# Optimization experiments

Measured on AMD Instinct MI355X. Metric: run time of the kernel, lower is better.

Reference implementation:

```python
import jax, jax.numpy as jnp
import numpy as np

N = 30        # samples per bezier curve
W = 60        # output image side
LENGTH = 160  # curves per sample
ALPHA = 2e-4  # gaussian splat bandwidth
VIEWBOX = (0.0, 0.0, 1.0, 1.0)
BATCH = 128


def _bezier_T(n):
    # matches the torch buffer: reparametrized t, then (reordered) Bernstein basis
    t = jnp.arange(n, dtype=jnp.float32) / n
    t = 2.0 * t**3 - 3.0 * t**2 + 2.0 * t
    t3 = t**3
    return jnp.stack([t3,
                      3.0 * (t**2 - t3),
                      3.0 * (t3 - 2.0 * t**2 + t),
                      (1.0 - t)**3], axis=1)  # [n, 4]


def setup_inputs() -> dict:
    key = jax.random.key(0)
    x = jax.random.uniform(key, (BATCH, LENGTH, 8), dtype=jnp.float32)
    return {"x": x}


def reference(x):
    B = x.shape[0]
    T = _bezier_T(N)                                   # [n, 4]
    board = jnp.arange(W, dtype=jnp.float32) / W       # [W]
    bX = board * VIEWBOX[2] + VIEWBOX[0]
    bY = board * VIEWBOX[3] + VIEWBOX[1]

    ctrl = x.reshape(B, LENGTH, 4, 2)
    pts = jnp.einsum('nk,blkc->blnc', T, ctrl)         # [B, L, n, 2] bezier samples
    X = pts[..., 0]                                    # [B, L, n]
    Y = pts[..., 1]

    # gaussian splat of each sampled point onto the pixel grid (separable)
    gX = jnp.exp(-jnp.square(bX[None, None, :, None] - X[:, :, None, :]) / ALPHA)  # [B, L, W, n]
    gY = jnp.exp(-jnp.square(bY[None, None, :, None] - Y[:, :, None, :]) / ALPHA)  # [B, L, W, n]

    # outer-product over the two axes, reduced over samples n and curves L
    res = jnp.einsum('blwn,blvn->bwv', gX, gY)         # [B, W, W]
    return jnp.minimum(res, 1.0)
```

## Files before the change

### kernel.cpp

```cpp
#include <hip/hip_runtime.h>


namespace {
constexpr int   kN = 30;
constexpr int   kW = 60;
constexpr int   kL = 160;
constexpr int   kB = 128;
constexpr float kAlphaInv = 5000.0f;
constexpr float kRadPix = 3.5f;
constexpr int   KSPLIT = 4;
constexpr int   CPB = kL / KSPLIT;
constexpr int   KPC = 32;
constexpr int   KBLK = CPB * KPC;
constexpr int   KC = 128;
constexpr int   NCH = KBLK / KC;
constexpr int   LDK = KC + 8;
constexpr int   kPix = kW * kW;
}

using f32x4 = __attribute__((ext_vector_type(4))) float;
using f16x8 = __attribute__((ext_vector_type(8))) _Float16;

__global__ __launch_bounds__(256, 2) void bezier_gemm_kernel(const float* __restrict__ x,
                                                             float* __restrict__ partial) {
  __shared__ _Float16 sh[2][64][LDK];
  const int b   = blockIdx.x / KSPLIT;
  const int ks  = blockIdx.x % KSPLIT;
  const int tid = threadIdx.x;
  const int lane = tid & 63;
  const int wid  = tid >> 6;
  const int wi = wid >> 1;
  const int vi = wid & 1;
  const int l15 = lane & 15;
  const int l4  = lane >> 4;

  f32x4 acc4[2][2] = {};

  const float* xb = x + ((size_t)b * kL + (size_t)ks * CPB) * 8;

  {
    uint4* shv = (uint4*)&sh[0][0][0];
    constexpr int NZ = 2 * 64 * LDK * 2 / 16;
    for (int i = tid; i < NZ; i += 256) shv[i] = make_uint4(0, 0, 0, 0);
  }

  const int col = tid & 127;
  const int mat = tid >> 7;
  const int n   = col & (KPC - 1);
  const bool valid = (n < kN);
  float B0, B1, B2, B3;
  {
    float t0 = (float)n * (1.0f / 30.0f);
    float t  = 2.0f * t0 * t0 * t0 - 3.0f * t0 * t0 + 2.0f * t0;
    float t2 = t * t, t3 = t2 * t;
    B0 = t3;
    B1 = 3.0f * (t2 - t3);
    B2 = 3.0f * (t3 - 2.0f * t2 + t);
    float omt = 1.0f - t;
    B3 = omt * omt * omt;
  }
  int lo_prev = 0;

  __syncthreads();

  for (int ch = 0; ch < NCH; ++ch) {
    if (valid) {
      const int lc = ch * 4 + (col >> 5);
      const float4* c = (const float4*)(xb + lc * 8);
      float4 c0 = c[0], c1 = c[1];
      float P = mat ? (B0 * c0.y + B1 * c0.w + B2 * c1.y + B3 * c1.w)
                    : (B0 * c0.x + B1 * c0.z + B2 * c1.x + B3 * c1.z);
      float fp = P * (float)kW;
      int lo = (int)ceilf(fp - kRadPix);
#pragma unroll
      for (int i = 0; i < 8; ++i) {
        int m = lo_prev + i;
        if (m >= 0 && m < kW) sh[mat][m][col] = (_Float16)0.0f;
      }
#pragma unroll
      for (int i = 0; i < 8; ++i) {
        int m = lo + i;
        float d = (float)m * (1.0f / 60.0f) - P;
        float e = __expf(-d * d * kAlphaInv);
        if (m >= 0 && m < kW) sh[mat][m][col] = (_Float16)e;
      }
      lo_prev = lo;
    }
    __syncthreads();

#pragma unroll
    for (int kk = 0; kk < KC; kk += 32) {
      const int ke = kk + l4 * 8;
      f16x8 a0 = *(const f16x8*)&sh[0][wi * 32 + l15][ke];
      f16x8 a1 = *(const f16x8*)&sh[0][wi * 32 + 16 + l15][ke];
      f16x8 b0 = *(const f16x8*)&sh[1][vi * 32 + l15][ke];
      f16x8 b1 = *(const f16x8*)&sh[1][vi * 32 + 16 + l15][ke];
      acc4[0][0] = __builtin_amdgcn_mfma_f32_16x16x32_f16(a0, b0, acc4[0][0], 0, 0, 0);
      acc4[0][1] = __builtin_amdgcn_mfma_f32_16x16x32_f16(a0, b1, acc4[0][1], 0, 0, 0);
      acc4[1][0] = __builtin_amdgcn_mfma_f32_16x16x32_f16(a1, b0, acc4[1][0], 0, 0, 0);
      acc4[1][1] = __builtin_amdgcn_mfma_f32_16x16x32_f16(a1, b1, acc4[1][1], 0, 0, 0);
    }
    __syncthreads();
  }

  float* pb = partial + (size_t)blockIdx.x * kPix;
#pragma unroll
  for (int mt = 0; mt < 2; ++mt) {
#pragma unroll
    for (int vt = 0; vt < 2; ++vt) {
      const int v = vi * 32 + vt * 16 + l15;
#pragma unroll
      for (int r = 0; r < 4; ++r) {
        const int w = wi * 32 + mt * 16 + l4 * 4 + r;
        if (w < kW && v < kW) pb[w * kW + v] = acc4[mt][vt][r];
      }
    }
  }
}

__global__ __launch_bounds__(256) void reduce_kernel(const float* __restrict__ partial,
                                                     float* __restrict__ out) {
  int i = blockIdx.x * 256 + threadIdx.x;
  if (i >= kB * kPix) return;
  int b = i / kPix;
  int j = i - b * kPix;
  const float* p = partial + (size_t)b * KSPLIT * kPix + j;
  float s = p[0] + p[kPix] + p[2 * kPix] + p[3 * kPix];
  out[i] = fminf(s, 1.0f);
}

__global__ __launch_bounds__(1024) void splat_direct_kernel(const float* __restrict__ x,
                                                            float* __restrict__ out) {
  __shared__ float res[kPix];
  const int b = blockIdx.x;
  const int tid = threadIdx.x;
  for (int i = tid; i < kPix; i += 1024) res[i] = 0.0f;
  __syncthreads();
  const float* xb = x + (size_t)b * kL * 8;
  for (int p = tid; p < kL * kN; p += 1024) {
    int l = p / kN;
    int n = p - l * kN;
    float t0 = (float)n * (1.0f / 30.0f);
    float t  = 2.0f * t0 * t0 * t0 - 3.0f * t0 * t0 + 2.0f * t0;
    float t2 = t * t, t3 = t2 * t;
    float B0 = t3, B1 = 3.0f * (t2 - t3), B2 = 3.0f * (t3 - 2.0f * t2 + t);
    float omt = 1.0f - t, B3 = omt * omt * omt;
    const float4* c = (const float4*)(xb + l * 8);
    float4 c0 = c[0], c1 = c[1];
    float X = B0 * c0.x + B1 * c0.z + B2 * c1.x + B3 * c1.z;
    float Y = B0 * c0.y + B1 * c0.w + B2 * c1.y + B3 * c1.w;
    float fx = X * kW, fy = Y * kW;
    int wlo = (int)ceilf(fx - kRadPix), vlo = (int)ceilf(fy - kRadPix);
    for (int i = 0; i < 8; ++i) {
      int w = wlo + i;
      if (w < 0 || w >= kW) continue;
      float dw = ((float)w - fx) * (1.0f / kW);
      float gx = __expf(-dw * dw * kAlphaInv);
      for (int j = 0; j < 8; ++j) {
        int v = vlo + j;
        if (v < 0 || v >= kW) continue;
        float dv = ((float)v - fy) * (1.0f / kW);
        atomicAdd(&res[w * kW + v], gx * __expf(-dv * dv * kAlphaInv));
      }
    }
  }
  __syncthreads();
  float* outb = out + (size_t)b * kPix;
  for (int i = tid; i < kPix; i += 1024) outb[i] = fminf(res[i], 1.0f);
}

extern "C" void kernel_launch(void* const* d_in, const int* in_sizes, int n_in,
                              void* d_out, int out_size, void* d_ws, size_t ws_size,
                              hipStream_t stream) {
  const float* x = (const float*)d_in[0];
  float* out = (float*)d_out;
  const size_t part_bytes = (size_t)kB * KSPLIT * kPix * sizeof(float);

  if (ws_size >= part_bytes) {
    float* partial = (float*)d_ws;
    bezier_gemm_kernel<<<dim3(kB * KSPLIT), dim3(256), 0, stream>>>(x, partial);
    int n = kB * kPix;
    reduce_kernel<<<dim3((n + 255) / 256), dim3(256), 0, stream>>>(partial, out);
  } else {
    splat_direct_kernel<<<dim3(kB), dim3(1024), 0, stream>>>(x, out);
  }
}
```

Measured before the change: 23.97 us.

## Fuse split-K GEMM and reduction into one block per batch with 32x32 MFMA

```diff
diff --git a/kernel.cpp b/kernel.cpp
--- a/kernel.cpp
+++ b/kernel.cpp
@@ -8,45 +8,37 @@
 constexpr int   kB = 128;
 constexpr float kAlphaInv = 5000.0f;
 constexpr float kRadPix = 3.5f;
-constexpr int   KSPLIT = 4;
-constexpr int   CPB = kL / KSPLIT;
-constexpr int   KPC = 32;
-constexpr int   KBLK = CPB * KPC;
-constexpr int   KC = 128;
-constexpr int   NCH = KBLK / KC;
-constexpr int   LDK = KC + 8;
+constexpr int   KC  = 256;
+constexpr int   NCH = kL * 32 / KC;
 constexpr int   kPix = kW * kW;
 }
 
-using f32x4 = __attribute__((ext_vector_type(4))) float;
-using f16x8 = __attribute__((ext_vector_type(8))) _Float16;
+using f32x16 = __attribute__((ext_vector_type(16))) float;
+using f16x8  = __attribute__((ext_vector_type(8))) _Float16;
 
-__global__ __launch_bounds__(256, 2) void bezier_gemm_kernel(const float* __restrict__ x,
-                                                             float* __restrict__ partial) {
-  __shared__ _Float16 sh[2][64][LDK];
-  const int b   = blockIdx.x / KSPLIT;
-  const int ks  = blockIdx.x % KSPLIT;
-  const int tid = threadIdx.x;
+__device__ __forceinline__ int lds_off(int mat, int row, int col) {
+  int g = ((col >> 3) ^ row) & 31;
+  g = ((col >> 3) & 24) | (((col >> 3) ^ row) & 7);
+  return ((mat << 6) + row) * KC + (g << 3) + (col & 7);
+}
+
+__global__ __launch_bounds__(512, 1) void bezier_fused_kernel(const float* __restrict__ x,
+                                                              float* __restrict__ out) {
+  __shared__ _Float16 sh[2 * 64 * KC];
+  const int b    = blockIdx.x;
+  const int tid  = threadIdx.x;
   const int lane = tid & 63;
   const int wid  = tid >> 6;
-  const int wi = wid >> 1;
-  const int vi = wid & 1;
-  const int l15 = lane & 15;
-  const int l4  = lane >> 4;
+  const int l31  = lane & 31;
+  const int hi   = lane >> 5;
 
-  f32x4 acc4[2][2] = {};
+  f32x16 acc[2][2] = {};
 
-  const float* xb = x + ((size_t)b * kL + (size_t)ks * CPB) * 8;
+  const float* xb = x + (size_t)b * kL * 8;
 
-  {
-    uint4* shv = (uint4*)&sh[0][0][0];
-    constexpr int NZ = 2 * 64 * LDK * 2 / 16;
-    for (int i = tid; i < NZ; i += 256) shv[i] = make_uint4(0, 0, 0, 0);
-  }
-
-  const int col = tid & 127;
-  const int mat = tid >> 7;
-  const int n   = col & (KPC - 1);
+  const int col = tid & 255;
+  const int mat = tid >> 8;
+  const int n   = col & 31;
   const bool valid = (n < kN);
   float B0, B1, B2, B3;
   {
@@ -59,13 +51,17 @@
     float omt = 1.0f - t;
     B3 = omt * omt * omt;
   }
-  int lo_prev = 0;
+  int lo_prev = -1000;
 
+  {
+    uint4* z = (uint4*)sh;
+    for (int i = tid; i < 2 * 64 * KC * 2 / 16; i += 512) z[i] = make_uint4(0, 0, 0, 0);
+  }
   __syncthreads();
 
   for (int ch = 0; ch < NCH; ++ch) {
     if (valid) {
-      const int lc = ch * 4 + (col >> 5);
+      const int lc = ch * 8 + (col >> 5);
       const float4* c = (const float4*)(xb + lc * 8);
       float4 c0 = c[0], c1 = c[1];
       float P = mat ? (B0 * c0.y + B1 * c0.w + B2 * c1.y + B3 * c1.w)
@@ -75,98 +71,77 @@
 #pragma unroll
       for (int i = 0; i < 8; ++i) {
         int m = lo_prev + i;
-        if (m >= 0 && m < kW) sh[mat][m][col] = (_Float16)0.0f;
+        if (m >= 0 && m < kW) sh[lds_off(mat, m, col)] = (_Float16)0.0f;
       }
 #pragma unroll
       for (int i = 0; i < 8; ++i) {
         int m = lo + i;
-        float d = (float)m * (1.0f / 60.0f) - P;
-        float e = __expf(-d * d * kAlphaInv);
-        if (m >= 0 && m < kW) sh[mat][m][col] = (_Float16)e;
+        if (m >= 0 && m < kW) {
+          float d = (float)m * (1.0f / 60.0f) - P;
+          sh[lds_off(mat, m, col)] = (_Float16)__expf(-d * d * kAlphaInv);
+        }
       }
       lo_prev = lo;
     }
     __syncthreads();
 
 #pragma unroll
-    for (int kk = 0; kk < KC; kk += 32) {
-      const int ke = kk + l4 * 8;
-      f16x8 a0 = *(const f16x8*)&sh[0][wi * 32 + l15][ke];
-      f16x8 a1 = *(const f16x8*)&sh[0][wi * 32 + 16 + l15][ke];
-      f16x8 b0 = *(const f16x8*)&sh[1][vi * 32 + l15][ke];
-      f16x8 b1 = *(const f16x8*)&sh[1][vi * 32 + 16 + l15][ke];
-      acc4[0][0] = __builtin_amdgcn_mfma_f32_16x16x32_f16(a0, b0, acc4[0][0], 0, 0, 0);
-      acc4[0][1] = __builtin_amdgcn_mfma_f32_16x16x32_f16(a0, b1, acc4[0][1], 0, 0, 0);
-      acc4[1][0] = __builtin_amdgcn_mfma_f32_16x16x32_f16(a1, b0, acc4[1][0], 0, 0, 0);
-      acc4[1][1] = __builtin_amdgcn_mfma_f32_16x16x32_f16(a1, b1, acc4[1][1], 0, 0, 0);
+    for (int ks = 0; ks < 2; ++ks) {
+      const int gb = wid * 4 + ks * 2 + hi;
+      const int ra = ((0 << 6) + l31) * KC + ((((gb ^ l31) & 7) | (gb & 24)) << 3);
+      const int rA = ((0 << 6) + 32 + l31) * KC + ((((gb ^ l31) & 7) | (gb & 24)) << 3);
+      const int rb = ((1 << 6) + l31) * KC + ((((gb ^ l31) & 7) | (gb & 24)) << 3);
+      const int rB = ((1 << 6) + 32 + l31) * KC + ((((gb ^ l31) & 7) | (gb & 24)) << 3);
+      f16x8 a0 = *(const f16x8*)&sh[ra];
+      f16x8 a1 = *(const f16x8*)&sh[rA];
+      f16x8 b0 = *(const f16x8*)&sh[rb];
+      f16x8 b1 = *(const f16x8*)&sh[rB];
+      acc[0][0] = __builtin_amdgcn_mfma_f32_32x32x16_f16(a0, b0, acc[0][0], 0, 0, 0);
+      acc[0][1] = __builtin_amdgcn_mfma_f32_32x32x16_f16(a0, b1, acc[0][1], 0, 0, 0);
+      acc[1][0] = __builtin_amdgcn_mfma_f32_32x32x16_f16(a1, b0, acc[1][0], 0, 0, 0);
+      acc[1][1] = __builtin_amdgcn_mfma_f32_32x32x16_f16(a1, b1, acc[1][1], 0, 0, 0);
     }
     __syncthreads();
   }
 
-  float* pb = partial + (size_t)blockIdx.x * kPix;
+  float* red = (float*)sh;
+  if (wid < 4) {
+    float* slot = red + wid * 4096;
 #pragma unroll
-  for (int mt = 0; mt < 2; ++mt) {
+    for (int mi = 0; mi < 2; ++mi)
 #pragma unroll
-    for (int vt = 0; vt < 2; ++vt) {
-      const int v = vi * 32 + vt * 16 + l15;
+      for (int vi = 0; vi < 2; ++vi)
 #pragma unroll
-      for (int r = 0; r < 4; ++r) {
-        const int w = wi * 32 + mt * 16 + l4 * 4 + r;
-        if (w < kW && v < kW) pb[w * kW + v] = acc4[mt][vt][r];
-      }
-    }
-  }
-}
-
-__global__ __launch_bounds__(256) void reduce_kernel(const float* __restrict__ partial,
-                                                     float* __restrict__ out) {
-  int i = blockIdx.x * 256 + threadIdx.x;
-  if (i >= kB * kPix) return;
-  int b = i / kPix;
-  int j = i - b * kPix;
-  const float* p = partial + (size_t)b * KSPLIT * kPix + j;
-  float s = p[0] + p[kPix] + p[2 * kPix] + p[3 * kPix];
-  out[i] = fminf(s, 1.0f);
-}
-
-__global__ __launch_bounds__(1024) void splat_direct_kernel(const float* __restrict__ x,
-                                                            float* __restrict__ out) {
-  __shared__ float res[kPix];
-  const int b = blockIdx.x;
-  const int tid = threadIdx.x;
-  for (int i = tid; i < kPix; i += 1024) res[i] = 0.0f;
-  __syncthreads();
-  const float* xb = x + (size_t)b * kL * 8;
-  for (int p = tid; p < kL * kN; p += 1024) {
-    int l = p / kN;
-    int n = p - l * kN;
-    float t0 = (float)n * (1.0f / 30.0f);
-    float t  = 2.0f * t0 * t0 * t0 - 3.0f * t0 * t0 + 2.0f * t0;
-    float t2 = t * t, t3 = t2 * t;
-    float B0 = t3, B1 = 3.0f * (t2 - t3), B2 = 3.0f * (t3 - 2.0f * t2 + t);
-    float omt = 1.0f - t, B3 = omt * omt * omt;
-    const float4* c = (const float4*)(xb + l * 8);
-    float4 c0 = c[0], c1 = c[1];
-    float X = B0 * c0.x + B1 * c0.z + B2 * c1.x + B3 * c1.z;
-    float Y = B0 * c0.y + B1 * c0.w + B2 * c1.y + B3 * c1.w;
-    float fx = X * kW, fy = Y * kW;
-    int wlo = (int)ceilf(fx - kRadPix), vlo = (int)ceilf(fy - kRadPix);
-    for (int i = 0; i < 8; ++i) {
-      int w = wlo + i;
-      if (w < 0 || w >= kW) continue;
-      float dw = ((float)w - fx) * (1.0f / kW);
-      float gx = __expf(-dw * dw * kAlphaInv);
-      for (int j = 0; j < 8; ++j) {
-        int v = vlo + j;
-        if (v < 0 || v >= kW) continue;
-        float dv = ((float)v - fy) * (1.0f / kW);
-        atomicAdd(&res[w * kW + v], gx * __expf(-dv * dv * kAlphaInv));
-      }
-    }
+        for (int r = 0; r < 16; ++r) {
+          int row = mi * 32 + (r & 3) + 8 * (r >> 2) + 4 * hi;
+          int cc  = vi * 32 + l31;
+          slot[row * 64 + cc] = acc[mi][vi][r];
+        }
   }
   __syncthreads();
-  float* outb = out + (size_t)b * kPix;
-  for (int i = tid; i < kPix; i += 1024) outb[i] = fminf(res[i], 1.0f);
+  if (wid >= 4) {
+    float* slot = red + (wid - 4) * 4096;
+#pragma unroll
+    for (int mi = 0; mi < 2; ++mi)
+#pragma unroll
+      for (int vi = 0; vi < 2; ++vi)
+#pragma unroll
+        for (int r = 0; r < 16; ++r) {
+          int row = mi * 32 + (r & 3) + 8 * (r >> 2) + 4 * hi;
+          int cc  = vi * 32 + l31;
+          slot[row * 64 + cc] += acc[mi][vi][r];
+        }
+  }
+  __syncthreads();
+
+  float* ob = out + (size_t)b * kPix;
+  for (int p = tid; p < kPix; p += 512) {
+    int r = p / kW;
+    int c = p - r * kW;
+    int idx = r * 64 + c;
+    float s = red[idx] + red[4096 + idx] + red[8192 + idx] + red[12288 + idx];
+    ob[p] = fminf(s, 1.0f);
+  }
 }
 
 extern "C" void kernel_launch(void* const* d_in, const int* in_sizes, int n_in,
@@ -174,14 +149,5 @@
                               hipStream_t stream) {
   const float* x = (const float*)d_in[0];
   float* out = (float*)d_out;
-  const size_t part_bytes = (size_t)kB * KSPLIT * kPix * sizeof(float);
-
-  if (ws_size >= part_bytes) {
-    float* partial = (float*)d_ws;
-    bezier_gemm_kernel<<<dim3(kB * KSPLIT), dim3(256), 0, stream>>>(x, partial);
-    int n = kB * kPix;
-    reduce_kernel<<<dim3((n + 255) / 256), dim3(256), 0, stream>>>(partial, out);
-  } else {
-    splat_direct_kernel<<<dim3(kB), dim3(1024), 0, stream>>>(x, out);
-  }
+  bezier_fused_kernel<<<dim3(kB), dim3(512), 0, stream>>>(x, out);
 }
```

Measured after the change: 31.66 us. +32.1%, slower.
